# Optimization experiments

Hardware: AMD Instinct MI355X
Metric: run time of the kernel (lower is better)

Reference implementation:

```python
import jax, jax.numpy as jnp
import numpy as np

B, C_IN, T, V = 32, 64, 300, 25
C_OUT = 128
INTER = max(8, C_IN // 2)
EPS = 1e-5


def setup_inputs() -> dict:
    key = jax.random.key(0)
    ks = jax.random.split(key, 9)
    s_in = 1.0 / np.sqrt(C_IN)
    return {
        "x": jax.random.normal(ks[0], (B, C_IN, T, V), dtype=jnp.float32),
        "theta_w": jax.random.uniform(ks[1], (INTER, C_IN), jnp.float32, -s_in, s_in),
        "theta_b": jax.random.uniform(ks[2], (INTER,), jnp.float32, -s_in, s_in),
        "phi_w": jax.random.uniform(ks[3], (INTER, C_IN), jnp.float32, -s_in, s_in),
        "phi_b": jax.random.uniform(ks[4], (INTER,), jnp.float32, -s_in, s_in),
        "g_w": jax.random.uniform(ks[5], (C_OUT, C_IN), jnp.float32, -s_in, s_in),
        "g_b": jax.random.uniform(ks[6], (C_OUT,), jnp.float32, -s_in, s_in),
        "bn_gamma": jnp.ones((C_OUT,), jnp.float32),
        "bn_beta": jnp.zeros((C_OUT,), jnp.float32),
    }


def reference(x, theta_w, theta_b, phi_w, phi_b, g_w, g_b, bn_gamma, bn_beta):
    # 1x1 convs == per-position linear projections over the channel dim
    th = jnp.einsum("bctv,ic->btvi", x, theta_w) + theta_b      # (B,T,V,inter)
    ph = jnp.einsum("bctv,ic->btiv", x, phi_w) + phi_b[None, None, :, None]  # (B,T,inter,V)
    # small-V non-local attention, per (b,t) slice
    scale = 1.0 / jnp.sqrt(jnp.asarray(INTER, x.dtype))
    A = jax.nn.softmax(jnp.einsum("btvi,btiw->btvw", th, ph) * scale, axis=-1)  # (B,T,V,V)
    g = jnp.einsum("bctv,oc->btvo", x, g_w) + g_b               # (B,T,V,out)
    out = jnp.einsum("btvw,btwo->btvo", A, g)                    # (B,T,V,out)
    out = jnp.transpose(out, (0, 3, 1, 2))                       # (B,out,T,V)
    # BatchNorm2d in training mode: batch stats over (B,T,V), biased variance
    mean = jnp.mean(out, axis=(0, 2, 3), keepdims=True)
    var = jnp.var(out, axis=(0, 2, 3), keepdims=True)
    out = (out - mean) * jax.lax.rsqrt(var + EPS)
    out = out * bn_gamma[None, :, None, None] + bn_beta[None, :, None, None]
    return out
```

## Files before the change

### kernel.cpp

```cpp
#include <hip/hip_runtime.h>

#define NB 32
#define CIN 64
#define TT 300
#define VV 25
#define CO 128
#define NSLICE 9600
#define NBLK 2400
#define NBUCKET 64
#define EPSV 1e-5f
#define SCALEV 0.17677669529663687f
#define NRED (NB*TT*VV)

using bf16x8 = __attribute__((ext_vector_type(8))) short;
using f32x4  = __attribute__((ext_vector_type(4))) float;
using f32x16 = __attribute__((ext_vector_type(16))) float;
typedef unsigned short ushort_t;

__device__ __forceinline__ unsigned short f2bf(float f) {
    union { float f; unsigned u; } v; v.f = f;
    unsigned u = v.u;
    return (unsigned short)((u + 0x7fffu + ((u >> 16) & 1u)) >> 16);
}

__device__ __forceinline__ unsigned pkbf(float a, float b) {
    unsigned r;
    asm("v_cvt_pk_bf16_f32 %0, %1, %2" : "=v"(r) : "v"(a), "v"(b));
    return r;
}

__device__ __forceinline__ void plswap(unsigned &a, unsigned &b) {
#if __has_builtin(__builtin_amdgcn_permlane32_swap)
    auto r = __builtin_amdgcn_permlane32_swap(a, b, false, false);
    a = r[0]; b = r[1];
#else
    unsigned a2, b2;
    asm("v_permlane32_swap_b32 %0, %1" : "=v"(a2), "=v"(b2) : "0"(a), "1"(b));
    a = a2; b = b2;
#endif
}
__device__ __forceinline__ float xhalf_sum(float x) {
    unsigned a = __float_as_uint(x), b = __float_as_uint(x);
    plswap(a, b);
    return __uint_as_float(a) + __uint_as_float(b);
}
__device__ __forceinline__ float xhalf_max(float x) {
    unsigned a = __float_as_uint(x), b = __float_as_uint(x);
    plswap(a, b);
    return fmaxf(__uint_as_float(a), __uint_as_float(b));
}
__device__ __forceinline__ f32x16 splat16(float v) {
    f32x16 r;
    #pragma unroll
    for (int i = 0; i < 16; ++i) r[i] = v;
    return r;
}

__device__ __forceinline__ void rearr(const f32x16& d, bf16x8& f0, bf16x8& f1) {
    unsigned u0 = pkbf(d[0],  d[1]),  u1 = pkbf(d[2],  d[3]);
    unsigned u2 = pkbf(d[4],  d[5]),  u3 = pkbf(d[6],  d[7]);
    unsigned u4 = pkbf(d[8],  d[9]),  u5 = pkbf(d[10], d[11]);
    unsigned u6 = pkbf(d[12], d[13]), u7 = pkbf(d[14], d[15]);
    plswap(u0, u2); plswap(u1, u3); plswap(u4, u6); plswap(u5, u7);
    union { unsigned u[4]; bf16x8 v; } c0, c1;
    c0.u[0] = u0; c0.u[1] = u1; c0.u[2] = u2; c0.u[3] = u3;
    c1.u[0] = u4; c1.u[1] = u5; c1.u[2] = u6; c1.u[3] = u7;
    f0 = c0.v; f1 = c1.v;
}

__global__ void agc_k0(const float* __restrict__ tw, const float* __restrict__ pw,
                       const float* __restrict__ gw,
                       const float* __restrict__ tb, const float* __restrict__ pb,
                       ushort_t* __restrict__ twA, ushort_t* __restrict__ pwA,
                       ushort_t* __restrict__ gwB,
                       float* __restrict__ tbD, float* __restrict__ pbD)
{
    int e = blockIdx.x*256 + threadIdx.x;
    if (e < 12288) {
        int j = e & 7, l = (e >> 3) & 63, ks = (e >> 9) & 3;
        int c = ks*16 + (l >> 5)*8 + j;
        int n = l & 31;
        int grp = e >> 11;
        if (grp == 0)      twA[e]        = f2bf(tw[n*CIN + c]);
        else if (grp == 1) pwA[e - 2048] = f2bf(pw[n*CIN + c]);
        else               gwB[e - 4096] = f2bf(gw[(grp - 2)*32*CIN + n*CIN + c]);
    } else if (e < 14336) {
        int e2 = e - 12288;
        int r = e2 & 15, l = (e2 >> 4) & 63;
        int i = (r & 3) + 8*(r >> 2) + 4*(l >> 5);
        if (e2 < 1024) tbD[e2]        = tb[i];
        else           pbD[e2 - 1024] = pb[i];
    }
}

__global__ __launch_bounds__(256) void agc_k1(
    const float* __restrict__ x, const float* __restrict__ gb,
    const ushort_t* __restrict__ twA, const ushort_t* __restrict__ pwA,
    const ushort_t* __restrict__ gwB,
    const float* __restrict__ tbD, const float* __restrict__ pbD,
    float* __restrict__ out, float* __restrict__ bsum, float* __restrict__ bsq)
{
    const int tid  = threadIdx.x;
    const int lane = tid & 63;
    const int wid  = tid >> 6;
    const int l31  = lane & 31;
    const int h    = lane >> 5;

    const int blk = blockIdx.x;
    const int sl  = ((blk & 7) * (NBLK/8) + (blk >> 3)) * 4 + wid;
    const int b   = sl / TT;
    const int t   = sl - b*TT;

    const float* xp = x + (size_t)b*CIN*TT*VV + (size_t)t*VV + (l31 < VV ? l31 : VV-1);
    bf16x8 xf[4];
    #pragma unroll
    for (int ks = 0; ks < 4; ++ks) {
        float v[8];
        #pragma unroll
        for (int j = 0; j < 8; ++j)
            v[j] = xp[(size_t)(ks*16 + h*8 + j)*TT*VV];
        union { unsigned u[4]; bf16x8 f; } c;
        c.u[0] = pkbf(v[0], v[1]); c.u[1] = pkbf(v[2], v[3]);
        c.u[2] = pkbf(v[4], v[5]); c.u[3] = pkbf(v[6], v[7]);
        xf[ks] = c.f;
    }

    f32x16 th, ph;
    #pragma unroll
    for (int r = 0; r < 4; ++r) {
        f32x4 bb = ((const f32x4*)(tbD + lane*16))[r];
        th[4*r+0] = bb[0]; th[4*r+1] = bb[1]; th[4*r+2] = bb[2]; th[4*r+3] = bb[3];
        f32x4 pp = ((const f32x4*)(pbD + lane*16))[r];
        ph[4*r+0] = pp[0]; ph[4*r+1] = pp[1]; ph[4*r+2] = pp[2]; ph[4*r+3] = pp[3];
    }
    #pragma unroll
    for (int ks = 0; ks < 4; ++ks) {
        bf16x8 twf = *(const bf16x8*)(twA + (ks*64 + lane)*8);
        th = __builtin_amdgcn_mfma_f32_32x32x16_bf16(twf, xf[ks], th, 0, 0, 0);
        bf16x8 pwf = *(const bf16x8*)(pwA + (ks*64 + lane)*8);
        ph = __builtin_amdgcn_mfma_f32_32x32x16_bf16(pwf, xf[ks], ph, 0, 0, 0);
    }

    bf16x8 thf0, thf1, phf0, phf1;
    rearr(th, thf0, thf1);
    rearr(ph, phf0, phf1);
    f32x16 st = splat16(0.f);
    st = __builtin_amdgcn_mfma_f32_32x32x16_bf16(phf0, thf0, st, 0, 0, 0);
    st = __builtin_amdgcn_mfma_f32_32x32x16_bf16(phf1, thf1, st, 0, 0, 0);

    float s[13];
    #pragma unroll
    for (int r = 0; r < 13; ++r) s[r] = st[r] * SCALEV;
    float m = fmaxf(fmaxf(fmaxf(s[0], s[1]), fmaxf(s[2], s[3])),
                    fmaxf(fmaxf(s[4], s[5]), fmaxf(s[6], s[7])));
    m = fmaxf(m, fmaxf(fmaxf(s[8], s[9]), fmaxf(s[10], s[11])));
    float s12 = h ? -3.4e38f : s[12];
    m = fmaxf(m, s12);
    m = xhalf_max(m);
    f32x16 pd;
    #pragma unroll
    for (int r = 0; r < 12; ++r) pd[r] = __expf(s[r] - m);
    pd[12] = h ? 0.f : __expf(s[12] - m);
    pd[13] = 0.f; pd[14] = 0.f; pd[15] = 0.f;
    float sum = ((pd[0]+pd[1]) + (pd[2]+pd[3])) + ((pd[4]+pd[5]) + (pd[6]+pd[7]))
              + ((pd[8]+pd[9]) + (pd[10]+pd[11])) + pd[12];
    sum = xhalf_sum(sum);
    float rinv;
    asm("v_rcp_f32 %0, %1" : "=v"(rinv) : "v"(sum));
    #pragma unroll
    for (int r = 0; r < 13; ++r) pd[r] *= rinv;
    bf16x8 pf0, pf1;
    rearr(pd, pf0, pf1);

    const int bkt = blk & (NBUCKET-1);
    float* opb = out + (size_t)b*CO*TT*VV + (size_t)t*VV + 4*h;
    #pragma unroll
    for (int ot = 0; ot < 4; ++ot) {
        f32x16 gd = splat16(0.f);
        #pragma unroll
        for (int ks = 0; ks < 4; ++ks) {
            bf16x8 gf = *(const bf16x8*)(gwB + ((ot*4 + ks)*64 + lane)*8);
            gd = __builtin_amdgcn_mfma_f32_32x32x16_bf16(xf[ks], gf, gd, 0, 0, 0);
        }
        bf16x8 gf0, gf1;
        rearr(gd, gf0, gf1);
        f32x16 od = splat16(gb[ot*32 + l31]);
        od = __builtin_amdgcn_mfma_f32_32x32x16_bf16(pf0, gf0, od, 0, 0, 0);
        od = __builtin_amdgcn_mfma_f32_32x32x16_bf16(pf1, gf1, od, 0, 0, 0);

        float* op = opb + (size_t)(ot*32 + l31)*TT*VV;
        float ss = 0.f, qq = 0.f;
        #pragma unroll
        for (int r = 0; r < 12; ++r) {
            int voff = (r & 3) + 8*(r >> 2);
            op[voff] = od[r];
            ss += od[r]; qq = fmaf(od[r], od[r], qq);
        }
        if (!h) {
            op[24] = od[12];
            ss += od[12]; qq = fmaf(od[12], od[12], qq);
        }
        ss = xhalf_sum(ss); qq = xhalf_sum(qq);
        if (lane < 32) {
            atomicAdd(&bsum[bkt*CO + ot*32 + l31], ss);
            atomicAdd(&bsq [bkt*CO + ot*32 + l31], qq);
        }
    }
}

__global__ void agc_k2(const float* __restrict__ bsum, const float* __restrict__ bsq,
                       const float* __restrict__ gamma, const float* __restrict__ beta,
                       float* __restrict__ scl, float* __restrict__ shf)
{
    const int o = threadIdx.x;
    float s = 0.f, q = 0.f;
    for (int k = 0; k < NBUCKET; ++k) { s += bsum[k*CO + o]; q += bsq[k*CO + o]; }
    float mean = s / (float)NRED;
    float var  = q / (float)NRED - mean*mean;
    float rstd = rsqrtf(var + EPSV);
    float sc = gamma[o] * rstd;
    scl[o] = sc;
    shf[o] = beta[o] - mean * sc;
}

__global__ __launch_bounds__(256) void agc_k3(
    float* __restrict__ out, const float* __restrict__ scl, const float* __restrict__ shf)
{
    const int n4 = NB*CO*TT*VV/4;
    float4* p = (float4*)out;
    for (int i = blockIdx.x*blockDim.x + threadIdx.x; i < n4; i += gridDim.x*blockDim.x) {
        int ch = (i / (TT*VV/4)) & (CO-1);
        float4 v = p[i];
        float sc = scl[ch], sh = shf[ch];
        v.x = fmaf(v.x, sc, sh);
        v.y = fmaf(v.y, sc, sh);
        v.z = fmaf(v.z, sc, sh);
        v.w = fmaf(v.w, sc, sh);
        p[i] = v;
    }
}

extern "C" void kernel_launch(void* const* d_in, const int* in_sizes, int n_in,
                              void* d_out, int out_size, void* d_ws, size_t ws_size,
                              hipStream_t stream) {
    const float* x     = (const float*)d_in[0];
    const float* tw    = (const float*)d_in[1];
    const float* tbb   = (const float*)d_in[2];
    const float* pw    = (const float*)d_in[3];
    const float* pbb   = (const float*)d_in[4];
    const float* gw    = (const float*)d_in[5];
    const float* gbb   = (const float*)d_in[6];
    const float* gamma = (const float*)d_in[7];
    const float* beta  = (const float*)d_in[8];
    float* out = (float*)d_out;
    float* ws  = (float*)d_ws;

    float* bsum = ws;
    float* bsq  = ws + NBUCKET*CO;
    float* scl  = ws + 2*NBUCKET*CO;
    float* shf  = ws + 2*NBUCKET*CO + CO;
    ushort_t* twA = (ushort_t*)(ws + 2*NBUCKET*CO + 2*CO);
    ushort_t* pwA = twA + 2048;
    ushort_t* gwB = twA + 4096;
    float* tbD = (float*)(gwB + 8192);
    float* pbD = tbD + 1024;

    hipMemsetAsync(d_ws, 0, (size_t)(2*NBUCKET*CO)*sizeof(float), stream);
    agc_k0<<<56, 256, 0, stream>>>(tw, pw, gw, tbb, pbb, twA, pwA, gwB, tbD, pbD);
    agc_k1<<<NBLK, 256, 0, stream>>>(x, gbb, twA, pwA, gwB, tbD, pbD, out, bsum, bsq);
    agc_k2<<<1, CO, 0, stream>>>(bsum, bsq, gamma, beta, scl, shf);
    agc_k3<<<2048, 256, 0, stream>>>(out, scl, shf);
}
```

Baseline: 106.8 us.

## Stage x loads and output stores through LDS for coalesced global access

Each block now loads its four (b,t) slices of x cooperatively as contiguous float4 rows into shared memory, and the waves read their operands from there instead of doing strided per-lane global loads. Outputs are written to a rotated (bank-conflict-avoiding) LDS tile and then copied out as contiguous float2 rows per channel, in two halves of 64 channels. BN partial sums are first reduced in LDS and then added with one global atomic per channel per block, which cuts global atomic traffic. The cost is extra barriers and LDS usage that may lower occupancy, and the output is staged in two rounds that serialise compute and stores.

```diff
diff --git a/kernel.cpp b/kernel.cpp
--- a/kernel.cpp
+++ b/kernel.cpp
@@ -5,7 +5,6 @@
 #define TT 300
 #define VV 25
 #define CO 128
-#define NSLICE 9600
 #define NBLK 2400
 #define NBUCKET 64
 #define EPSV 1e-5f
@@ -22,13 +21,11 @@
     unsigned u = v.u;
     return (unsigned short)((u + 0x7fffu + ((u >> 16) & 1u)) >> 16);
 }
-
 __device__ __forceinline__ unsigned pkbf(float a, float b) {
     unsigned r;
     asm("v_cvt_pk_bf16_f32 %0, %1, %2" : "=v"(r) : "v"(a), "v"(b));
     return r;
 }
-
 __device__ __forceinline__ void plswap(unsigned &a, unsigned &b) {
 #if __has_builtin(__builtin_amdgcn_permlane32_swap)
     auto r = __builtin_amdgcn_permlane32_swap(a, b, false, false);
@@ -55,7 +52,6 @@
     for (int i = 0; i < 16; ++i) r[i] = v;
     return r;
 }
-
 __device__ __forceinline__ void rearr(const f32x16& d, bf16x8& f0, bf16x8& f1) {
     unsigned u0 = pkbf(d[0],  d[1]),  u1 = pkbf(d[2],  d[3]);
     unsigned u2 = pkbf(d[4],  d[5]),  u3 = pkbf(d[6],  d[7]);
@@ -100,6 +96,11 @@
     const float* __restrict__ tbD, const float* __restrict__ pbD,
     float* __restrict__ out, float* __restrict__ bsum, float* __restrict__ bsq)
 {
+    __shared__ __align__(16) float lds[6656];
+    float* xs   = lds;
+    float* outS = lds;
+    float* red  = lds + 6400;
+
     const int tid  = threadIdx.x;
     const int lane = tid & 63;
     const int wid  = tid >> 6;
@@ -107,23 +108,34 @@
     const int h    = lane >> 5;
 
     const int blk = blockIdx.x;
-    const int sl  = ((blk & 7) * (NBLK/8) + (blk >> 3)) * 4 + wid;
-    const int b   = sl / TT;
-    const int t   = sl - b*TT;
-
-    const float* xp = x + (size_t)b*CIN*TT*VV + (size_t)t*VV + (l31 < VV ? l31 : VV-1);
+    const int grp = (blk & 7) * (NBLK/8) + (blk >> 3);
+    const int b   = grp / 75;
+    const int j4  = grp - b*75;
+
+    red[tid] = 0.f;
+
+    const float4* gx = (const float4*)x + (size_t)b*120000 + (size_t)j4*25;
+    for (int e = tid; e < 1600; e += 256) {
+        int c = e / 25, q = e - c*25;
+        *(float4*)&xs[c*100 + q*4] = gx[c*1875 + q];
+    }
+    __syncthreads();
+
+    const int vcl  = l31 < VV ? l31 : VV-1;
+    const int colx = wid*25 + vcl;
     bf16x8 xf[4];
     #pragma unroll
     for (int ks = 0; ks < 4; ++ks) {
         float v[8];
         #pragma unroll
-        for (int j = 0; j < 8; ++j)
-            v[j] = xp[(size_t)(ks*16 + h*8 + j)*TT*VV];
+        for (int jj = 0; jj < 8; ++jj)
+            v[jj] = xs[(ks*16 + h*8 + jj)*100 + colx];
         union { unsigned u[4]; bf16x8 f; } c;
         c.u[0] = pkbf(v[0], v[1]); c.u[1] = pkbf(v[2], v[3]);
         c.u[2] = pkbf(v[4], v[5]); c.u[3] = pkbf(v[6], v[7]);
         xf[ks] = c.f;
     }
+    __syncthreads();
 
     f32x16 th, ph;
     #pragma unroll
@@ -172,10 +184,9 @@
     bf16x8 pf0, pf1;
     rearr(pd, pf0, pf1);
 
-    const int bkt = blk & (NBUCKET-1);
-    float* opb = out + (size_t)b*CO*TT*VV + (size_t)t*VV + 4*h;
-    #pragma unroll
-    for (int ot = 0; ot < 4; ++ot) {
+    const int sv0 = wid*25 + 4*h;
+
+    auto process_ot = [&](int ot) {
         f32x16 gd = splat16(0.f);
         #pragma unroll
         for (int ks = 0; ks < 4; ++ks) {
@@ -188,23 +199,56 @@
         od = __builtin_amdgcn_mfma_f32_32x32x16_bf16(pf0, gf0, od, 0, 0, 0);
         od = __builtin_amdgcn_mfma_f32_32x32x16_bf16(pf1, gf1, od, 0, 0, 0);
 
-        float* op = opb + (size_t)(ot*32 + l31)*TT*VV;
+        const int o_loc = (ot & 1)*32 + l31;
+        const int base  = o_loc*100;
         float ss = 0.f, qq = 0.f;
         #pragma unroll
         for (int r = 0; r < 12; ++r) {
-            int voff = (r & 3) + 8*(r >> 2);
-            op[voff] = od[r];
+            int sv = sv0 + (r & 3) + 8*(r >> 2);
+            int u  = (sv >> 1) + o_loc;
+            if (u >= 50) u -= 50;
+            if (u >= 50) u -= 50;
+            outS[base + u*2 + (sv & 1)] = od[r];
             ss += od[r]; qq = fmaf(od[r], od[r], qq);
         }
         if (!h) {
-            op[24] = od[12];
+            int sv = wid*25 + 24;
+            int u  = (sv >> 1) + o_loc;
+            if (u >= 50) u -= 50;
+            if (u >= 50) u -= 50;
+            outS[base + u*2 + (sv & 1)] = od[12];
             ss += od[12]; qq = fmaf(od[12], od[12], qq);
         }
         ss = xhalf_sum(ss); qq = xhalf_sum(qq);
         if (lane < 32) {
-            atomicAdd(&bsum[bkt*CO + ot*32 + l31], ss);
-            atomicAdd(&bsq [bkt*CO + ot*32 + l31], qq);
-        }
+            atomicAdd(&red[ot*32 + l31], ss);
+            atomicAdd(&red[128 + ot*32 + l31], qq);
+        }
+    };
+
+    auto readback = [&](int p) {
+        float2* o2 = (float2*)out;
+        for (int e = tid; e < 3200; e += 256) {
+            int ol = e / 50, q2 = e - ol*50;
+            int u = q2 + ol;
+            if (u >= 50) u -= 50;
+            if (u >= 50) u -= 50;
+            float2 v = *(float2*)&outS[ol*100 + u*2];
+            o2[(size_t)(b*CO + p*64 + ol)*3750 + (size_t)j4*50 + q2] = v;
+        }
+    };
+
+    process_ot(0); process_ot(1);
+    __syncthreads();
+    readback(0);
+    __syncthreads();
+    process_ot(2); process_ot(3);
+    __syncthreads();
+    readback(1);
+    if (tid < CO) {
+        int bkt = blk & (NBUCKET-1);
+        atomicAdd(&bsum[bkt*CO + tid], red[tid]);
+        atomicAdd(&bsq [bkt*CO + tid], red[128 + tid]);
     }
 }
 
@@ -214,6 +258,7 @@
 {
     const int o = threadIdx.x;
     float s = 0.f, q = 0.f;
+    #pragma unroll 8
     for (int k = 0; k < NBUCKET; ++k) { s += bsum[k*CO + o]; q += bsq[k*CO + o]; }
     float mean = s / (float)NRED;
     float var  = q / (float)NRED - mean*mean;
```

After: 105.4 us. No clear change (-1.3%).
